# Kernel tuning notes

Hardware: AMD Instinct MI355X
Metric: run time of the kernel (lower is better)

The kernel has to match this reference:

```python
import jax, jax.numpy as jnp
import numpy as np

N_QUBITS = 4


def _apply_rx(state, theta, wire):
    # state: [B, 2,2,2,2] complex64, theta: [B] real angles; RX on `wire`.
    st = jnp.moveaxis(state, wire + 1, -1)
    bshape = (theta.shape[0],) + (1,) * (st.ndim - 2)
    c = jnp.cos(theta * 0.5).reshape(bshape).astype(jnp.complex64)
    s = (-1j) * jnp.sin(theta * 0.5).reshape(bshape).astype(jnp.complex64)
    new = jnp.stack([c * st[..., 0] + s * st[..., 1],
                     s * st[..., 0] + c * st[..., 1]], axis=-1)
    return jnp.moveaxis(new, -1, wire + 1)


def _apply_cnot(state, control, target):
    st = jnp.moveaxis(state, (control + 1, target + 1), (-2, -1))
    new = jnp.stack([st[..., 0, :], st[..., 1, ::-1]], axis=-2)
    return jnp.moveaxis(new, (-2, -1), (control + 1, target + 1))


def _quantum_gate(angles, thetas):
    # angles: [B, n] data-encoding RX angles; thetas: [n] trainable RX angles.
    B, n = angles.shape
    state = jnp.zeros((B,) + (2,) * n, jnp.complex64)
    state = state.at[(slice(None),) + (0,) * n].set(1.0)  # |0...0>
    for w in range(n):
        state = _apply_rx(state, angles[:, w], w)
    for w in range(n):
        state = _apply_rx(state, jnp.broadcast_to(thetas[w], (B,)), w)
    for w in range(n):
        state = _apply_cnot(state, w, (w + 1) % n)
    probs = jnp.abs(state.reshape(B, 2 ** n)) ** 2  # [B, 16]
    bits = (np.arange(2 ** n)[:, None] >> np.arange(n - 1, -1, -1)[None, :]) & 1
    signs = jnp.asarray(1.0 - 2.0 * bits, jnp.float32)  # [16, n] PauliZ eigvals
    return probs @ signs  # [B, n] <Z_w> expectations


def setup_inputs() -> dict:
    key = jax.random.key(0)
    ks = jax.random.split(key, 12)
    B, D, H, n = 131072, 256, 4, N_QUBITS
    fan_in = D + H
    sc = 1.0 / np.sqrt(fan_in)
    inp = {
        'x': jax.random.normal(ks[0], (B, D), jnp.float32),
        'hx': jax.random.normal(ks[1], (B, H), jnp.float32),
        'cx': jax.random.normal(ks[2], (B, H), jnp.float32),
        'W_f': jax.random.normal(ks[3], (n, fan_in), jnp.float32) * sc,
        'b_f': jnp.zeros((n,), jnp.float32),
        'W_i': jax.random.normal(ks[4], (n, fan_in), jnp.float32) * sc,
        'b_i': jnp.zeros((n,), jnp.float32),
        'W_u': jax.random.normal(ks[5], (n, fan_in), jnp.float32) * sc,
        'b_u': jnp.zeros((n,), jnp.float32),
        'W_o': jax.random.normal(ks[6], (n, fan_in), jnp.float32) * sc,
        'b_o': jnp.zeros((n,), jnp.float32),
        'th_f': jax.random.normal(ks[7], (n,), jnp.float32),
        'th_i': jax.random.normal(ks[8], (n,), jnp.float32),
        'th_u': jax.random.normal(ks[9], (n,), jnp.float32),
        'th_o': jax.random.normal(ks[10], (n,), jnp.float32),
    }
    return inp


def reference(x, hx, cx, W_f, b_f, W_i, b_i, W_u, b_u, W_o, b_o,
              th_f, th_i, th_u, th_o):
    comb = jnp.concatenate([x, hx], axis=1)  # [B, D+H]
    f = jax.nn.sigmoid(_quantum_gate(comb @ W_f.T + b_f, th_f))
    i = jax.nn.sigmoid(_quantum_gate(comb @ W_i.T + b_i, th_i))
    g = jnp.tanh(_quantum_gate(comb @ W_u.T + b_u, th_u))
    o = jax.nn.sigmoid(_quantum_gate(comb @ W_o.T + b_o, th_o))
    c_new = f * cx + i * g
    h_new = o * jnp.tanh(c_new)
    return (h_new, c_new)
```

## Files before the change

### kernel.cpp

```cpp
#include <hip/hip_runtime.h>

#define NB    131072
#define TPB   64
#define FANIN 260
#define SROWF4 9

__device__ __forceinline__ float sigm_(float x) { return 1.0f / (1.0f + __expf(-x)); }
__device__ __forceinline__ float tanh_(float x) { return 1.0f - 2.0f / (__expf(2.0f * x) + 1.0f); }

__global__ void qlstm_prep(const float* __restrict__ Wf, const float* __restrict__ bf,
                           const float* __restrict__ Wi, const float* __restrict__ bi,
                           const float* __restrict__ Wu, const float* __restrict__ bu,
                           const float* __restrict__ Wo, const float* __restrict__ bo,
                           const float* __restrict__ thf, const float* __restrict__ thi,
                           const float* __restrict__ thu, const float* __restrict__ tho,
                           float* __restrict__ Wp, float* __restrict__ bth) {
    int t = blockIdx.x * blockDim.x + threadIdx.x;
    if (t < FANIN * 16) {
        int k = t >> 4, gw = t & 15, g = gw >> 2, w = gw & 3;
        const float* Wg = (g == 0) ? Wf : (g == 1) ? Wi : (g == 2) ? Wu : Wo;
        Wp[t] = Wg[w * FANIN + k];
    }
    if (t < 16) {
        int g = t >> 2, w = t & 3;
        const float* bg = (g == 0) ? bf  : (g == 1) ? bi  : (g == 2) ? bu  : bo;
        const float* tg = (g == 0) ? thf : (g == 1) ? thi : (g == 2) ? thu : tho;
        bth[t] = bg[w] + tg[w];
    }
}

__global__ __launch_bounds__(TPB) void qlstm_main(
        const float* __restrict__ x, const float* __restrict__ hx,
        const float* __restrict__ cx, const float* __restrict__ Wp,
        const float* __restrict__ bth, float* __restrict__ out) {
    __shared__ float4 xs4[2 * TPB * SROWF4];

    const int lane = threadIdx.x;
    const int row0 = blockIdx.x * TPB;
    const int row  = row0 + lane;

    const float4* x4 = (const float4*)x;

    float4 hv  = ((const float4*)hx)[row];
    float4 cxv = ((const float4*)cx)[row];

    float4 pf[8];
#pragma unroll
    for (int u = 0; u < 8; ++u) {
        int f = lane + (u << 6);
        pf[u] = x4[(size_t)(row0 + (f >> 3)) * 64 + (f & 7)];
    }
#pragma unroll
    for (int u = 0; u < 8; ++u) {
        int f = lane + (u << 6);
        xs4[(f >> 3) * SROWF4 + (f & 7)] = pf[u];
    }

    float acc[16];
#pragma unroll
    for (int j = 0; j < 16; ++j) acc[j] = 0.0f;

#pragma unroll 2
    for (int stage = 0; stage < 8; ++stage) {
        float4* cur = &xs4[(stage & 1)        * (TPB * SROWF4)];
        float4* nxt = &xs4[((stage + 1) & 1)  * (TPB * SROWF4)];

        if (stage < 7) {
#pragma unroll
            for (int u = 0; u < 8; ++u) {
                int f = lane + (u << 6);
                pf[u] = x4[(size_t)(row0 + (f >> 3)) * 64 + (stage + 1) * 8 + (f & 7)];
            }
        }

        float4 xr[8];
#pragma unroll
        for (int k4 = 0; k4 < 8; ++k4) xr[k4] = cur[lane * SROWF4 + k4];

        const float* wbase = Wp + stage * 32 * 16;
#pragma unroll
        for (int k4 = 0; k4 < 8; ++k4) {
#pragma unroll
            for (int m = 0; m < 4; ++m) {
                float xe = (m == 0) ? xr[k4].x : (m == 1) ? xr[k4].y
                         : (m == 2) ? xr[k4].z : xr[k4].w;
                const float* wp = wbase + (k4 * 4 + m) * 16;
#pragma unroll
                for (int j = 0; j < 16; ++j) acc[j] = fmaf(xe, wp[j], acc[j]);
            }
        }

        if (stage < 7) {
#pragma unroll
            for (int u = 0; u < 8; ++u) {
                int f = lane + (u << 6);
                nxt[(f >> 3) * SROWF4 + (f & 7)] = pf[u];
            }
        }
    }

    {
        const float* wp = Wp + 256 * 16;
#pragma unroll
        for (int j = 0; j < 16; ++j) acc[j] = fmaf(hv.x, wp[j],      acc[j]);
#pragma unroll
        for (int j = 0; j < 16; ++j) acc[j] = fmaf(hv.y, wp[16 + j], acc[j]);
#pragma unroll
        for (int j = 0; j < 16; ++j) acc[j] = fmaf(hv.z, wp[32 + j], acc[j]);
#pragma unroll
        for (int j = 0; j < 16; ++j) acc[j] = fmaf(hv.w, wp[48 + j], acc[j]);
    }

    float co[16];
#pragma unroll
    for (int j = 0; j < 16; ++j) co[j] = __cosf(acc[j] + bth[j]);

    float G[16];
#pragma unroll
    for (int g = 0; g < 4; ++g) {
        float c0 = co[g * 4 + 0], c1 = co[g * 4 + 1];
        float c2 = co[g * 4 + 2], c3 = co[g * 4 + 3];
        float e1 = c0 * c1;
        float e2 = e1 * c2;
        float e3 = e2 * c3;
        float e0 = c1 * c2 * c3;
        G[g * 4 + 0] = e0; G[g * 4 + 1] = e1; G[g * 4 + 2] = e2; G[g * 4 + 3] = e3;
    }

    float cxa[4] = {cxv.x, cxv.y, cxv.z, cxv.w};
    float hn[4], cn[4];
#pragma unroll
    for (int w = 0; w < 4; ++w) {
        float fg = sigm_(G[0 * 4 + w]);
        float ig = sigm_(G[1 * 4 + w]);
        float ug = tanh_(G[2 * 4 + w]);
        float og = sigm_(G[3 * 4 + w]);
        float c_ = fg * cxa[w] + ig * ug;
        cn[w] = c_;
        hn[w] = og * tanh_(c_);
    }

    ((float4*)out)[row]      = make_float4(hn[0], hn[1], hn[2], hn[3]);
    ((float4*)out)[NB + row] = make_float4(cn[0], cn[1], cn[2], cn[3]);
}

extern "C" void kernel_launch(void* const* d_in, const int* in_sizes, int n_in,
                              void* d_out, int out_size, void* d_ws, size_t ws_size,
                              hipStream_t stream) {
    const float* x   = (const float*)d_in[0];
    const float* hx  = (const float*)d_in[1];
    const float* cx  = (const float*)d_in[2];
    const float* Wf  = (const float*)d_in[3];
    const float* bf  = (const float*)d_in[4];
    const float* Wi  = (const float*)d_in[5];
    const float* bi  = (const float*)d_in[6];
    const float* Wu  = (const float*)d_in[7];
    const float* bu  = (const float*)d_in[8];
    const float* Wo  = (const float*)d_in[9];
    const float* bo  = (const float*)d_in[10];
    const float* thf = (const float*)d_in[11];
    const float* thi = (const float*)d_in[12];
    const float* thu = (const float*)d_in[13];
    const float* tho = (const float*)d_in[14];

    float* Wp  = (float*)d_ws;
    float* bth = Wp + FANIN * 16;

    qlstm_prep<<<(FANIN * 16 + 255) / 256, 256, 0, stream>>>(
        Wf, bf, Wi, bi, Wu, bu, Wo, bo, thf, thi, thu, tho, Wp, bth);

    qlstm_main<<<NB / TPB, TPB, 0, stream>>>(
        x, hx, cx, Wp, bth, (float*)d_out);
}
```

Measured before the change: 274.8 us.

## Stream x tiles directly into LDS via global_load_lds with XOR swizzle

```diff
diff --git a/kernel.cpp b/kernel.cpp
--- a/kernel.cpp
+++ b/kernel.cpp
@@ -3,10 +3,15 @@
 #define NB    131072
 #define TPB   64
 #define FANIN 260
-#define SROWF4 9
 
 __device__ __forceinline__ float sigm_(float x) { return 1.0f / (1.0f + __expf(-x)); }
 __device__ __forceinline__ float tanh_(float x) { return 1.0f - 2.0f / (__expf(2.0f * x) + 1.0f); }
+
+__device__ __forceinline__ void gld_lds16(const float4* gsrc, float4* ldst) {
+    __builtin_amdgcn_global_load_lds(
+        (const __attribute__((address_space(1))) void*)gsrc,
+        (__attribute__((address_space(3))) void*)ldst, 16, 0, 0);
+}
 
 __global__ void qlstm_prep(const float* __restrict__ Wf, const float* __restrict__ bf,
                            const float* __restrict__ Wi, const float* __restrict__ bi,
@@ -29,32 +34,27 @@
     }
 }
 
-__global__ __launch_bounds__(TPB) void qlstm_main(
+__global__ __launch_bounds__(TPB, 2) void qlstm_main(
         const float* __restrict__ x, const float* __restrict__ hx,
         const float* __restrict__ cx, const float* __restrict__ Wp,
         const float* __restrict__ bth, float* __restrict__ out) {
-    __shared__ float4 xs4[2 * TPB * SROWF4];
+    __shared__ float4 xs4[2 * TPB * 8];
 
     const int lane = threadIdx.x;
     const int row0 = blockIdx.x * TPB;
     const int row  = row0 + lane;
-
     const float4* x4 = (const float4*)x;
 
     float4 hv  = ((const float4*)hx)[row];
     float4 cxv = ((const float4*)cx)[row];
 
-    float4 pf[8];
+    const int rsub = lane >> 3;
+    const int csw  = (lane & 7) ^ rsub;
+    const size_t gbase = (size_t)(row0 + rsub) * 64 + csw;
+
 #pragma unroll
-    for (int u = 0; u < 8; ++u) {
-        int f = lane + (u << 6);
-        pf[u] = x4[(size_t)(row0 + (f >> 3)) * 64 + (f & 7)];
-    }
-#pragma unroll
-    for (int u = 0; u < 8; ++u) {
-        int f = lane + (u << 6);
-        xs4[(f >> 3) * SROWF4 + (f & 7)] = pf[u];
-    }
+    for (int u = 0; u < 8; ++u)
+        gld_lds16(x4 + gbase + (size_t)u * 8 * 64, &xs4[u * 64]);
 
     float acc[16];
 #pragma unroll
@@ -62,39 +62,30 @@
 
 #pragma unroll 2
     for (int stage = 0; stage < 8; ++stage) {
-        float4* cur = &xs4[(stage & 1)        * (TPB * SROWF4)];
-        float4* nxt = &xs4[((stage + 1) & 1)  * (TPB * SROWF4)];
+        const int cb = (stage & 1) * (TPB * 8);
 
         if (stage < 7) {
+            const int nb_ = ((stage + 1) & 1) * (TPB * 8);
 #pragma unroll
-            for (int u = 0; u < 8; ++u) {
-                int f = lane + (u << 6);
-                pf[u] = x4[(size_t)(row0 + (f >> 3)) * 64 + (stage + 1) * 8 + (f & 7)];
-            }
+            for (int u = 0; u < 8; ++u)
+                gld_lds16(x4 + gbase + (size_t)(stage + 1) * 8 + (size_t)u * 8 * 64,
+                          &xs4[nb_ + u * 64]);
+            asm volatile("s_waitcnt vmcnt(8)" ::: "memory");
+        } else {
+            asm volatile("s_waitcnt vmcnt(0)" ::: "memory");
         }
-
-        float4 xr[8];
-#pragma unroll
-        for (int k4 = 0; k4 < 8; ++k4) xr[k4] = cur[lane * SROWF4 + k4];
 
         const float* wbase = Wp + stage * 32 * 16;
 #pragma unroll
         for (int k4 = 0; k4 < 8; ++k4) {
+            float4 xv = xs4[cb + lane * 8 + (k4 ^ (lane & 7))];
 #pragma unroll
             for (int m = 0; m < 4; ++m) {
-                float xe = (m == 0) ? xr[k4].x : (m == 1) ? xr[k4].y
-                         : (m == 2) ? xr[k4].z : xr[k4].w;
+                float xe = (m == 0) ? xv.x : (m == 1) ? xv.y
+                         : (m == 2) ? xv.z : xv.w;
                 const float* wp = wbase + (k4 * 4 + m) * 16;
 #pragma unroll
                 for (int j = 0; j < 16; ++j) acc[j] = fmaf(xe, wp[j], acc[j]);
-            }
-        }
-
-        if (stage < 7) {
-#pragma unroll
-            for (int u = 0; u < 8; ++u) {
-                int f = lane + (u << 6);
-                nxt[(f >> 3) * SROWF4 + (f & 7)] = pf[u];
             }
         }
     }
```

New measurement: 241.2 us. 1.14x faster.
